# Kernel tuning notes

Measured on AMD Instinct MI355X. Metric: run time of the kernel, lower is better.

The kernel has to match this reference:

```python
import jax, jax.numpy as jnp
import numpy as np

D_MODEL = 1024
N_HEADS = 16
D_HEAD = 64
SEQ = 2048
BATCH = 2
ATTN_SCALE = float(np.sqrt(D_HEAD))  # cfg.use_attn_scale = True
NEG_INF = -1e9


def setup_inputs() -> dict:
    key = jax.random.key(0)
    ks = jax.random.split(key, 8)
    s = 0.02
    return {
        "query_input": jax.random.normal(ks[0], (BATCH, SEQ, D_MODEL), jnp.float32),
        "key_input": jax.random.normal(ks[1], (BATCH, SEQ, D_MODEL), jnp.float32),
        "value_input": jax.random.normal(ks[2], (BATCH, SEQ, D_MODEL), jnp.float32),
        "W_Q": jax.random.normal(ks[3], (N_HEADS, D_MODEL, D_HEAD), jnp.float32) * s,
        "W_K": jax.random.normal(ks[4], (N_HEADS, D_MODEL, D_HEAD), jnp.float32) * s,
        "W_V": jax.random.normal(ks[5], (N_HEADS, D_MODEL, D_HEAD), jnp.float32) * s,
        "W_O": jax.random.normal(ks[6], (N_HEADS, D_HEAD, D_MODEL), jnp.float32) * s,
        "b_Q": jnp.zeros((N_HEADS, D_HEAD), jnp.float32),
        "b_K": jnp.zeros((N_HEADS, D_HEAD), jnp.float32),
        "b_V": jnp.zeros((N_HEADS, D_HEAD), jnp.float32),
        "b_O": jnp.zeros((D_MODEL,), jnp.float32),
    }


def reference(query_input, key_input, value_input, W_Q, W_K, W_V, W_O, b_Q, b_K, b_V, b_O):
    # QKV projections: [batch, pos, d_model] x [head, d_model, d_head] -> [batch, pos, head, d_head]
    q = jnp.einsum("bpd,hde->bphe", query_input, W_Q) + b_Q
    k = jnp.einsum("bpd,hde->bphe", key_input, W_K) + b_K
    v = jnp.einsum("bpd,hde->bphe", value_input, W_V) + b_V

    # attn scores [batch, head, query_pos, key_pos]
    scores = jnp.einsum("bqhe,bkhe->bhqk", q, k) / ATTN_SCALE

    # causal mask (attn_type == 'global'): tril over [n_ctx, n_ctx] sliced to seq
    causal = jnp.tril(jnp.ones((SEQ, SEQ), bool))
    scores = jnp.where(causal[None, None, :, :], scores, NEG_INF)

    pattern = jax.nn.softmax(scores, axis=-1)

    # z: [batch, query_pos, head, d_head]
    z = jnp.einsum("bhqk,bkhe->bqhe", pattern, v)

    # output projection: [batch, pos, d_model]
    out = jnp.einsum("bqhe,hed->bqd", z, W_O) + b_O
    return out
```

## Files before the change

kernel.cpp:

```cpp
#include <hip/hip_runtime.h>
#include <stdint.h>


typedef __attribute__((ext_vector_type(8))) short short8;
typedef __attribute__((ext_vector_type(4))) short short4v;
typedef __attribute__((ext_vector_type(4))) float floatx4;
typedef __attribute__((ext_vector_type(4))) unsigned int uintx4;
typedef __attribute__((ext_vector_type(2))) unsigned int uint2v;

#define MFMA16(a, b, c) __builtin_amdgcn_mfma_f32_16x16x32_bf16(a, b, c, 0, 0, 0)

#if __has_builtin(__builtin_amdgcn_mfma_f32_16x16x16bf16_1k)
#define HAVE_K16 1
#define MFMAK16(a, b, c) __builtin_amdgcn_mfma_f32_16x16x16bf16_1k(a, b, c, 0, 0, 0)
#else
#define HAVE_K16 0
#endif

__device__ __forceinline__ unsigned short f2b(float f) {
  unsigned int u = __builtin_bit_cast(unsigned int, f);
  u = (u + 0x7fffu + ((u >> 16) & 1u)) >> 16;
  return (unsigned short)u;
}
__device__ __forceinline__ float exp2f_fast(float x) {
#if __has_builtin(__builtin_amdgcn_exp2f)
  return __builtin_amdgcn_exp2f(x);
#else
  return exp2f(x);
#endif
}
__device__ __forceinline__ unsigned int pack2_bf16(float lo, float hi) {
#if __has_builtin(__builtin_amdgcn_perm)
  return __builtin_amdgcn_perm(__builtin_bit_cast(unsigned int, hi),
                               __builtin_bit_cast(unsigned int, lo), 0x07060302u);
#else
  return (__builtin_bit_cast(unsigned int, lo) >> 16) |
         (__builtin_bit_cast(unsigned int, hi) & 0xffff0000u);
#endif
}

__device__ __forceinline__ void async_copy16(void* lds, const void* g) {
  __builtin_amdgcn_global_load_lds(
      (const __attribute__((address_space(1))) unsigned int*)g,
      (__attribute__((address_space(3))) unsigned int*)lds, 16, 0, 0);
}

__device__ __forceinline__ void xpose4(floatx4& v, int lane) {
  {
    float s0 = __shfl_xor(v[1], 1, 64);
    float s1 = __shfl_xor(v[0], 1, 64);
    float s2 = __shfl_xor(v[3], 1, 64);
    float s3 = __shfl_xor(v[2], 1, 64);
    if (lane & 1) { v[0] = s0; v[2] = s2; } else { v[1] = s1; v[3] = s3; }
  }
  {
    float s0 = __shfl_xor(v[2], 2, 64);
    float s1 = __shfl_xor(v[3], 2, 64);
    float s2 = __shfl_xor(v[0], 2, 64);
    float s3 = __shfl_xor(v[1], 2, 64);
    if (lane & 2) { v[0] = s0; v[1] = s1; } else { v[2] = s2; v[3] = s3; }
  }
}

__global__ __launch_bounds__(256) void convall(
    const float* __restrict__ Xq, const float* __restrict__ Xk,
    const float* __restrict__ Xv, const float* __restrict__ WQ,
    const float* __restrict__ WK, const float* __restrict__ WV,
    const float* __restrict__ WO, unsigned short* __restrict__ xout,
    unsigned short* __restrict__ wout, unsigned short* __restrict__ woout) {
  __shared__ float T[64][65];
  const int bid = blockIdx.x;
  const int t = threadIdx.x;
  if (bid < 12288) {
    const int yy = bid / 4096, x = bid - yy * 4096;
    const float* in = (yy == 0) ? Xq : ((yy == 1) ? Xk : Xv);
    size_t i = (size_t)x * 256 + t;
    float4 v = ((const float4*)in)[i];
    ushort4 u;
    u.x = f2b(v.x); u.y = f2b(v.y); u.z = f2b(v.z); u.w = f2b(v.w);
    ((ushort4*)(xout + (size_t)yy * 4194304))[i] = u;
    return;
  }
  const int rr = t >> 4, cc = t & 15;
  if (bid < 13056) {
    const int sub = bid - 12288;
    const int yy = sub >> 8, x = sub & 255;
    const float* in = (yy == 0) ? WQ : ((yy == 1) ? WK : WV);
    const int h = x >> 4, d0 = (x & 15) << 6;
#pragma unroll
    for (int it = 0; it < 4; ++it) {
      int dl = it * 16 + rr;
      float4 v = *(const float4*)&in[(size_t)h * 65536 + (size_t)(d0 + dl) * 64 + cc * 4];
      T[dl][cc * 4 + 0] = v.x; T[dl][cc * 4 + 1] = v.y;
      T[dl][cc * 4 + 2] = v.z; T[dl][cc * 4 + 3] = v.w;
    }
    __syncthreads();
    unsigned short* ob = wout + (size_t)yy * 1048576;
#pragma unroll
    for (int it = 0; it < 4; ++it) {
      int e = it * 16 + rr;
      ushort4 u;
      u.x = f2b(T[cc * 4 + 0][e]); u.y = f2b(T[cc * 4 + 1][e]);
      u.z = f2b(T[cc * 4 + 2][e]); u.w = f2b(T[cc * 4 + 3][e]);
      *(ushort4*)&ob[(size_t)(h * 64 + e) * 1024 + d0 + cc * 4] = u;
    }
    return;
  }
  {
    const int x = bid - 13056;
    const int r0 = (x & 15) << 6, c0 = (x >> 4) << 6;
#pragma unroll
    for (int it = 0; it < 4; ++it) {
      int rl = it * 16 + rr;
      float4 v = *(const float4*)&WO[(size_t)(r0 + rl) * 1024 + c0 + cc * 4];
      T[rl][cc * 4 + 0] = v.x; T[rl][cc * 4 + 1] = v.y;
      T[rl][cc * 4 + 2] = v.z; T[rl][cc * 4 + 3] = v.w;
    }
    __syncthreads();
#pragma unroll
    for (int it = 0; it < 4; ++it) {
      int dl = it * 16 + rr;
      ushort4 u;
      u.x = f2b(T[cc * 4 + 0][dl]); u.y = f2b(T[cc * 4 + 1][dl]);
      u.z = f2b(T[cc * 4 + 2][dl]); u.w = f2b(T[cc * 4 + 3][dl]);
      *(ushort4*)&woout[(size_t)(c0 + dl) * 1024 + r0 + cc * 4] = u;
    }
  }
}

template <int TM, int NZ>
__global__ __launch_bounds__(512, (TM == 128) ? 6 : 4) void gemm512(
    const short* __restrict__ A0, const short* __restrict__ A1,
    const short* __restrict__ A2, const short* __restrict__ B0,
    const short* __restrict__ B1, const short* __restrict__ B2,
    const float* __restrict__ bias0, const float* __restrict__ bias1,
    const float* __restrict__ bias2, unsigned short* __restrict__ ob0,
    unsigned short* __restrict__ ob1, unsigned short* __restrict__ ob2,
    float* __restrict__ outf, float qscale) {
  constexpr int WAVES_N = (TM == 128) ? 2 : 4;
  constexpr int NJ = (TM == 128) ? 4 : 2;
  constexpr int NY = 4096 / TM;
  __shared__ short As[TM * 32];
  __shared__ short Bs[128 * 32];

  const int L = blockIdx.x;
  const int x = L / (NY * NZ);
  const int r = L - x * (NY * NZ);
  const int y = r / NZ;
  const int z = r - y * NZ;

  const short* A = (z == 0) ? A0 : (z == 1) ? A1 : A2;
  const short* Bt = (z == 0) ? B0 : (z == 1) ? B1 : B2;

  const int tid = threadIdx.x;
  const int lane = tid & 63, w = tid >> 6;
  const int quad = lane >> 4, col = lane & 15;
  const int m0 = y * TM, n0 = x * 128;
  const int wm = (w / WAVES_N) * 32, wn = (w % WAVES_N) * (NJ * 16);

  floatx4 acc[2][NJ] = {};

  const int lr = lane >> 2, gc = (lane & 3) ^ ((lane >> 3) & 3);
  const short* ga = A + (size_t)(m0 + w * 16 + lr) * 1024 + gc * 8;
  const short* gb = Bt + (size_t)(n0 + w * 16 + lr) * 1024 + gc * 8;
  const int asw = (col >> 1) & 3;
  const bool stageA = (w < TM / 16);

  for (int k0 = 0; k0 < 1024; k0 += 32) {
    if (stageA) async_copy16(&As[(w * 16) * 32], ga);
    async_copy16(&Bs[(w * 16) * 32], gb);
    ga += 32; gb += 32;
    __syncthreads();
    short8 af[2], bf[NJ];
#pragma unroll
    for (int mi = 0; mi < 2; ++mi)
      af[mi] = *(const short8*)&As[(wm + mi * 16 + col) * 32 + ((quad ^ asw) * 8)];
#pragma unroll
    for (int nj = 0; nj < NJ; ++nj)
      bf[nj] = *(const short8*)&Bs[(wn + nj * 16 + col) * 32 + ((quad ^ asw) * 8)];
#pragma unroll
    for (int mi = 0; mi < 2; ++mi)
#pragma unroll
      for (int nj = 0; nj < NJ; ++nj)
        acc[mi][nj] = MFMA16(af[mi], bf[nj], acc[mi][nj]);
    __syncthreads();
  }

  const float* bias = (z == 0) ? bias0 : (z == 1) ? bias1 : bias2;
  unsigned short* outb = (z == 0) ? ob0 : (z == 1) ? ob1 : ob2;
  const int mode = (NZ == 3) ? ((z == 2) ? 2 : 1) : 0;
  const float scale = (NZ == 3 && z == 0) ? qscale : 1.0f;

  float bv[NJ];
#pragma unroll
  for (int nj = 0; nj < NJ; ++nj) bv[nj] = bias[n0 + wn + nj * 16 + col];

  if (mode == 2) {
#pragma unroll
    for (int mi = 0; mi < 2; ++mi)
#pragma unroll
      for (int nj = 0; nj < NJ; ++nj) {
        int m = m0 + wm + mi * 16 + quad * 4;
        int n = n0 + wn + nj * 16 + col;
        int bb = m >> 11, s = m & 2047, h = n >> 6, e = n & 63;
        ushort4 u;
        u.x = f2b(acc[mi][nj][0] + bv[nj]);
        u.y = f2b(acc[mi][nj][1] + bv[nj]);
        u.z = f2b(acc[mi][nj][2] + bv[nj]);
        u.w = f2b(acc[mi][nj][3] + bv[nj]);
        *(ushort4*)&outb[(((size_t)bb * 16 + h) * 64 + e) * 2048 + s] = u;
      }
  } else {
#pragma unroll
    for (int mi = 0; mi < 2; ++mi)
#pragma unroll
      for (int nj = 0; nj < NJ; ++nj) {
        floatx4 v;
#pragma unroll
        for (int rr = 0; rr < 4; ++rr) v[rr] = (acc[mi][nj][rr] + bv[nj]) * scale;
        xpose4(v, lane);
        int m = m0 + wm + mi * 16 + quad * 4 + (col & 3);
        int nb = n0 + wn + nj * 16 + (col & ~3);
        if (mode == 0) {
          *(floatx4*)&outf[(size_t)m * 1024 + nb] = v;
        } else {
          int bb = m >> 11, s = m & 2047, h = nb >> 6, e = nb & 63;
          ushort4 u;
          u.x = f2b(v[0]); u.y = f2b(v[1]); u.z = f2b(v[2]); u.w = f2b(v[3]);
          *(ushort4*)&outb[(((size_t)bb * 16 + h) * 2048 + s) * 64 + e] = u;
        }
      }
  }
}

#if !HAVE_K16
__device__ __forceinline__ void exchange4(const unsigned int* u01,
                                          const unsigned int* u23, int srcA,
                                          int srcB, bool hiq, short8& pf0,
                                          short8& pf1) {
  unsigned int xA0 = (unsigned int)__shfl((int)u01[0], srcA, 64);
  unsigned int xA1 = (unsigned int)__shfl((int)u01[1], srcA, 64);
  unsigned int yA0 = (unsigned int)__shfl((int)u23[0], srcA, 64);
  unsigned int yA1 = (unsigned int)__shfl((int)u23[1], srcA, 64);
  unsigned int xB0 = (unsigned int)__shfl((int)u01[0], srcB, 64);
  unsigned int xB1 = (unsigned int)__shfl((int)u01[1], srcB, 64);
  unsigned int yB0 = (unsigned int)__shfl((int)u23[0], srcB, 64);
  unsigned int yB1 = (unsigned int)__shfl((int)u23[1], srcB, 64);
  uintx4 v0;
  v0.x = hiq ? xA1 : xA0; v0.y = hiq ? yA1 : yA0;
  v0.z = hiq ? xB1 : xB0; v0.w = hiq ? yB1 : yB0;
  pf0 = __builtin_bit_cast(short8, v0);
  xA0 = (unsigned int)__shfl((int)u01[2], srcA, 64);
  xA1 = (unsigned int)__shfl((int)u01[3], srcA, 64);
  yA0 = (unsigned int)__shfl((int)u23[2], srcA, 64);
  yA1 = (unsigned int)__shfl((int)u23[3], srcA, 64);
  xB0 = (unsigned int)__shfl((int)u01[2], srcB, 64);
  xB1 = (unsigned int)__shfl((int)u01[3], srcB, 64);
  yB0 = (unsigned int)__shfl((int)u23[2], srcB, 64);
  yB1 = (unsigned int)__shfl((int)u23[3], srcB, 64);
  uintx4 v1;
  v1.x = hiq ? xA1 : xA0; v1.y = hiq ? yA1 : yA0;
  v1.z = hiq ? xB1 : xB0; v1.w = hiq ? yB1 : yB0;
  pf1 = __builtin_bit_cast(short8, v1);
}
#endif

__device__ __forceinline__ void stage_kv(short* Kbuf, short* Vbuf,
                                         const short* kg, const short* vg,
                                         int kv0, int w, int slr, int sgc) {
  const short* kr = kg + (size_t)(kv0 + w * 16 + slr) * 64 + sgc * 8;
  async_copy16(&Kbuf[(w * 16) * 64], kr);
  async_copy16(&Kbuf[(w * 16 + 8) * 64], kr + 8 * 64);
  const short* vr = vg + (size_t)(w * 16 + slr) * 2048 + kv0 + sgc * 8;
  async_copy16(&Vbuf[(w * 16) * 64], vr);
  async_copy16(&Vbuf[(w * 16 + 8) * 64], vr + 8 * 2048);
}

__global__ __launch_bounds__(256) void attn(const short* __restrict__ q,
                                            const short* __restrict__ k,
                                            const short* __restrict__ vt,
                                            unsigned short* __restrict__ z) {
  __shared__ short Ks[2][64 * 64];
  __shared__ short Vs[2][64 * 64];

  const int tid = threadIdx.x;
  const int lane = tid & 63, w = tid >> 6;
  const int quad = lane >> 4, col = lane & 15;
  const int qt = 31 - (blockIdx.x >> 5), bh = blockIdx.x & 31;
  const int q0 = qt * 64, qw0 = q0 + w * 16;
  const size_t base = (size_t)bh * (2048 * 64);

  const short* qp = q + base + (size_t)(qw0 + col) * 64 + quad * 8;
  short8 bq0 = *(const short8*)qp;
  short8 bq1 = *(const short8*)(qp + 32);

  floatx4 o[4] = {};
  float m_run = -1e30f, l_run = 0.f;

  const short* kg = k + base;
  const short* vg = vt + base;
  const int ksw = col & 7;
  const int slr = lane >> 3, sgc = (lane & 7) ^ slr;
#if !HAVE_K16
  const int srcA = ((quad & 1) << 5) + col, srcB = srcA + 16;
  const bool hiq = (quad & 2) != 0;
#endif

  stage_kv(Ks[0], Vs[0], kg, vg, 0, w, slr, sgc);
  int p = 0;

  for (int t = 0; t <= qt; ++t) {
    __syncthreads();
    if (t < qt) stage_kv(Ks[p ^ 1], Vs[p ^ 1], kg, vg, (t + 1) * 64, w, slr, sgc);

    const bool diag = (t == qt);
    const int mtmax = diag ? w : 3;

    floatx4 st[4];
#pragma unroll
    for (int mt = 0; mt < 4; ++mt) {
      if (mt <= mtmax) {
        const short* kb = &Ks[p][(mt * 16 + col) * 64];
        short8 ka0 = *(const short8*)(kb + (quad ^ ksw) * 8);
        short8 ka1 = *(const short8*)(kb + ((quad + 4) ^ ksw) * 8);
        floatx4 a = {0.f, 0.f, 0.f, 0.f};
        a = MFMA16(ka0, bq0, a);
        a = MFMA16(ka1, bq1, a);
        if (diag && mt == mtmax) {
#pragma unroll
          for (int r = 0; r < 4; ++r)
            if (quad * 4 + r > col) a[r] = -1e9f;
        }
        st[mt] = a;
      }
    }

    float pmax = -3e38f;
#pragma unroll
    for (int mt = 0; mt < 4; ++mt)
      if (mt <= mtmax) {
#pragma unroll
        for (int r = 0; r < 4; ++r) pmax = fmaxf(pmax, st[mt][r]);
      }
    pmax = fmaxf(pmax, __shfl_xor(pmax, 16, 64));
    pmax = fmaxf(pmax, __shfl_xor(pmax, 32, 64));
    float mnew = fmaxf(m_run, pmax);
    float alpha = exp2f_fast(m_run - mnew);
    m_run = mnew;

    unsigned int u01[4], u23[4];
    float lsum = 0.f;
#pragma unroll
    for (int mt = 0; mt < 4; ++mt) {
      if (mt <= mtmax) {
        float p0 = exp2f_fast(st[mt][0] - mnew);
        float p1 = exp2f_fast(st[mt][1] - mnew);
        float p2 = exp2f_fast(st[mt][2] - mnew);
        float p3 = exp2f_fast(st[mt][3] - mnew);
        lsum += (p0 + p1) + (p2 + p3);
        u01[mt] = pack2_bf16(p0, p1);
        u23[mt] = pack2_bf16(p2, p3);
      } else {
        u01[mt] = 0u; u23[mt] = 0u;
      }
    }
    lsum += __shfl_xor(lsum, 16, 64);
    lsum += __shfl_xor(lsum, 32, 64);
    l_run = l_run * alpha + lsum;

#if HAVE_K16
    short4v pb[4];
#pragma unroll
    for (int mt = 0; mt < 4; ++mt) {
      uint2v uu;
      uu.x = u01[mt]; uu.y = u23[mt];
      pb[mt] = __builtin_bit_cast(short4v, uu);
    }
#pragma unroll
    for (int et = 0; et < 4; ++et) {
      const short* vrow = &Vs[p][(et * 16 + col) * 64];
      floatx4 t0 = o[et];
#pragma unroll
      for (int r = 0; r < 4; ++r) t0[r] *= alpha;
#pragma unroll
      for (int mt = 0; mt < 4; ++mt) {
        if (mt <= mtmax) {
          int c = mt * 2 + (quad >> 1);
          short4v va = *(const short4v*)&vrow[((c ^ ksw) * 8) + (quad & 1) * 4];
          t0 = MFMAK16(va, pb[mt], t0);
        }
      }
      o[et] = t0;
    }
#else
    short8 pf0, pf1;
    exchange4(u01, u23, srcA, srcB, hiq, pf0, pf1);
#pragma unroll
    for (int et = 0; et < 4; ++et) {
      const short* vb = &Vs[p][(et * 16 + col) * 64];
      short8 va0 = *(const short8*)(vb + (quad ^ ksw) * 8);
      short8 va1 = *(const short8*)(vb + ((quad + 4) ^ ksw) * 8);
      floatx4 t0 = o[et];
#pragma unroll
      for (int r = 0; r < 4; ++r) t0[r] *= alpha;
      t0 = MFMA16(va0, pf0, t0);
      t0 = MFMA16(va1, pf1, t0);
      o[et] = t0;
    }
#endif
    p ^= 1;
  }

  const int b = bh >> 4, h = bh & 15;
#if __has_builtin(__builtin_amdgcn_rcpf)
  const float invl = __builtin_amdgcn_rcpf(l_run);
#else
  const float invl = 1.f / l_run;
#endif
  unsigned short* zr = z + (((size_t)b * 2048 + qw0 + col) * 16 + h) * 64;
#pragma unroll
  for (int et = 0; et < 4; ++et) {
    ushort4 u;
    u.x = f2b(o[et][0] * invl); u.y = f2b(o[et][1] * invl);
    u.z = f2b(o[et][2] * invl); u.w = f2b(o[et][3] * invl);
    *(ushort4*)&zr[et * 16 + quad * 4] = u;
  }
}

extern "C" void kernel_launch(void* const* d_in, const int* in_sizes, int n_in,
                              void* d_out, int out_size, void* d_ws, size_t ws_size,
                              hipStream_t stream) {
  (void)in_sizes; (void)n_in; (void)out_size; (void)ws_size;
  const float* Xq = (const float*)d_in[0];
  const float* Xk = (const float*)d_in[1];
  const float* Xv = (const float*)d_in[2];
  const float* WQ = (const float*)d_in[3];
  const float* WK = (const float*)d_in[4];
  const float* WV = (const float*)d_in[5];
  const float* WO = (const float*)d_in[6];
  const float* bQ = (const float*)d_in[7];
  const float* bK = (const float*)d_in[8];
  const float* bV = (const float*)d_in[9];
  const float* bO = (const float*)d_in[10];
  float* out = (float*)d_out;

  unsigned short* xqb = (unsigned short*)d_ws;
  unsigned short* xkb = xqb + 4194304;
  unsigned short* xvb = xkb + 4194304;
  unsigned short* wqt = xvb + 4194304;
  unsigned short* wkt = wqt + 1048576;
  unsigned short* wvt = wkt + 1048576;
  unsigned short* wot = wvt + 1048576;
  unsigned short* qb = wot + 1048576;
  unsigned short* kb = qb + 4194304;
  unsigned short* vtb = kb + 4194304;
  unsigned short* zb = vtb + 4194304;

  convall<<<13312, 256, 0, stream>>>(Xq, Xk, Xv, WQ, WK, WV, WO, xqb, wqt, wot);

  const float qscale = 0.125f * 1.44269504088896f;
  gemm512<128, 3><<<768, 512, 0, stream>>>(
      (const short*)xqb, (const short*)xkb, (const short*)xvb,
      (const short*)wqt, (const short*)wkt, (const short*)wvt, bQ, bK, bV, qb,
      kb, vtb, nullptr, qscale);

  attn<<<1024, 256, 0, stream>>>((const short*)qb, (const short*)kb,
                                 (const short*)vtb, zb);

  gemm512<64, 1><<<512, 512, 0, stream>>>(
      (const short*)zb, (const short*)zb, (const short*)zb, (const short*)wot,
      (const short*)wot, (const short*)wot, bO, bO, bO, nullptr, nullptr,
      nullptr, out, 1.0f);
}
```

Baseline: 218.9 us.

## Pair causal query tiles per block to share K/V staging and balance work

Each attention block now processes two query tiles (pr and 31-pr) of the same head, so every block covers 33 KV steps and work is balanced across the causal triangle. The staged K/V tiles are reused by both query tiles, which roughly halves K/V shared-memory loads per query. It also skips the online-softmax rescale when the running max does not change for the whole wavefront. The cost is halving the grid to 512 blocks and higher register pressure from two accumulator sets, which may reduce occupancy.

```diff
diff --git a/kernel.cpp b/kernel.cpp
--- a/kernel.cpp
+++ b/kernel.cpp
@@ -276,6 +276,117 @@
   async_copy16(&Vbuf[(w * 16 + 8) * 64], vr + 8 * 2048);
 }
 
+__device__ __forceinline__ void attn_step(const short* __restrict__ Kp,
+                                          const short* __restrict__ Vp,
+                                          const short8& bq0, const short8& bq1,
+                                          floatx4 (&o)[4], float& m_run,
+                                          float& l_run, int mtmax, bool diag) {
+  const int lane = threadIdx.x & 63;
+  const int quad = lane >> 4, col = lane & 15;
+  const int ksw = col & 7;
+
+  floatx4 st[4];
+#pragma unroll
+  for (int mt = 0; mt < 4; ++mt) {
+    if (mt <= mtmax) {
+      const short* kb = &Kp[(mt * 16 + col) * 64];
+      short8 ka0 = *(const short8*)(kb + (quad ^ ksw) * 8);
+      short8 ka1 = *(const short8*)(kb + ((quad + 4) ^ ksw) * 8);
+      floatx4 a = {0.f, 0.f, 0.f, 0.f};
+      a = MFMA16(ka0, bq0, a);
+      a = MFMA16(ka1, bq1, a);
+      if (diag && mt == mtmax) {
+#pragma unroll
+        for (int r = 0; r < 4; ++r)
+          if (quad * 4 + r > col) a[r] = -1e9f;
+      }
+      st[mt] = a;
+    }
+  }
+
+  float pmax = -3e38f;
+#pragma unroll
+  for (int mt = 0; mt < 4; ++mt)
+    if (mt <= mtmax) {
+#pragma unroll
+      for (int r = 0; r < 4; ++r) pmax = fmaxf(pmax, st[mt][r]);
+    }
+  pmax = fmaxf(pmax, __shfl_xor(pmax, 16, 64));
+  pmax = fmaxf(pmax, __shfl_xor(pmax, 32, 64));
+
+  const bool norescale = (__all(pmax <= m_run) != 0);
+  const float mnew = norescale ? m_run : fmaxf(m_run, pmax);
+  const float alpha = norescale ? 1.0f : exp2f_fast(m_run - mnew);
+  m_run = mnew;
+
+  unsigned int u01[4], u23[4];
+  float lsum = 0.f;
+#pragma unroll
+  for (int mt = 0; mt < 4; ++mt) {
+    if (mt <= mtmax) {
+      float p0 = exp2f_fast(st[mt][0] - mnew);
+      float p1 = exp2f_fast(st[mt][1] - mnew);
+      float p2 = exp2f_fast(st[mt][2] - mnew);
+      float p3 = exp2f_fast(st[mt][3] - mnew);
+      lsum += (p0 + p1) + (p2 + p3);
+      u01[mt] = pack2_bf16(p0, p1);
+      u23[mt] = pack2_bf16(p2, p3);
+    } else {
+      u01[mt] = 0u; u23[mt] = 0u;
+    }
+  }
+  lsum += __shfl_xor(lsum, 16, 64);
+  lsum += __shfl_xor(lsum, 32, 64);
+  l_run = norescale ? (l_run + lsum) : (l_run * alpha + lsum);
+
+#if HAVE_K16
+  short4v pb[4];
+#pragma unroll
+  for (int mt = 0; mt < 4; ++mt) {
+    uint2v uu;
+    uu.x = u01[mt]; uu.y = u23[mt];
+    pb[mt] = __builtin_bit_cast(short4v, uu);
+  }
+#pragma unroll
+  for (int et = 0; et < 4; ++et) {
+    const short* vrow = &Vp[(et * 16 + col) * 64];
+    floatx4 t0 = o[et];
+    if (!norescale) {
+#pragma unroll
+      for (int r = 0; r < 4; ++r) t0[r] *= alpha;
+    }
+#pragma unroll
+    for (int mt = 0; mt < 4; ++mt) {
+      if (mt <= mtmax) {
+        int c = mt * 2 + (quad >> 1);
+        short4v va = *(const short4v*)&vrow[((c ^ ksw) * 8) + (quad & 1) * 4];
+        t0 = MFMAK16(va, pb[mt], t0);
+      }
+    }
+    o[et] = t0;
+  }
+#else
+  const int srcA = ((quad & 1) << 5) + col, srcB = srcA + 16;
+  const bool hiq = (quad & 2) != 0;
+  short8 pf0, pf1;
+  exchange4(u01, u23, srcA, srcB, hiq, pf0, pf1);
+#pragma unroll
+  for (int et = 0; et < 4; ++et) {
+    const short* vb = &Vp[(et * 16 + col) * 64];
+    short8 va0 = *(const short8*)(vb + (quad ^ ksw) * 8);
+    short8 va1 = *(const short8*)(vb + ((quad + 4) ^ ksw) * 8);
+    floatx4 t0 = o[et];
+    if (!norescale) {
+#pragma unroll
+      for (int r = 0; r < 4; ++r) t0[r] *= alpha;
+    }
+    t0 = MFMA16(va0, pf0, t0);
+    t0 = MFMA16(va1, pf1, t0);
+    o[et] = t0;
+  }
+#endif
+}
+
 __global__ __launch_bounds__(256) void attn(const short* __restrict__ q,
                                             const short* __restrict__ k,
                                             const short* __restrict__ vt,
@@ -286,144 +397,66 @@
   const int tid = threadIdx.x;
   const int lane = tid & 63, w = tid >> 6;
   const int quad = lane >> 4, col = lane & 15;
-  const int qt = 31 - (blockIdx.x >> 5), bh = blockIdx.x & 31;
-  const int q0 = qt * 64, qw0 = q0 + w * 16;
+
+  const int bb = blockIdx.x;
+  const int bh = bb & 31;
+  const int pr = (bb < 256) ? (bb >> 5) : (15 - ((bb - 256) >> 5));
+  const int qtA = pr, qtB = 31 - pr;
+  const int q0A = qtA * 64, q0B = qtB * 64;
   const size_t base = (size_t)bh * (2048 * 64);
 
-  const short* qp = q + base + (size_t)(qw0 + col) * 64 + quad * 8;
-  short8 bq0 = *(const short8*)qp;
-  short8 bq1 = *(const short8*)(qp + 32);
-
-  floatx4 o[4] = {};
-  float m_run = -1e30f, l_run = 0.f;
+  const short* qpA = q + base + (size_t)(q0A + w * 16 + col) * 64 + quad * 8;
+  short8 bq0A = *(const short8*)qpA;
+  short8 bq1A = *(const short8*)(qpA + 32);
+  const short* qpB = q + base + (size_t)(q0B + w * 16 + col) * 64 + quad * 8;
+  short8 bq0B = *(const short8*)qpB;
+  short8 bq1B = *(const short8*)(qpB + 32);
+
+  floatx4 oA[4] = {}, oB[4] = {};
+  float mA = -1e30f, lA = 0.f;
+  float mB = -1e30f, lB = 0.f;
 
   const short* kg = k + base;
   const short* vg = vt + base;
-  const int ksw = col & 7;
   const int slr = lane >> 3, sgc = (lane & 7) ^ slr;
-#if !HAVE_K16
-  const int srcA = ((quad & 1) << 5) + col, srcB = srcA + 16;
-  const bool hiq = (quad & 2) != 0;
-#endif
 
   stage_kv(Ks[0], Vs[0], kg, vg, 0, w, slr, sgc);
   int p = 0;
 
-  for (int t = 0; t <= qt; ++t) {
+  for (int t = 0; t <= qtB; ++t) {
     __syncthreads();
-    if (t < qt) stage_kv(Ks[p ^ 1], Vs[p ^ 1], kg, vg, (t + 1) * 64, w, slr, sgc);
-
-    const bool diag = (t == qt);
-    const int mtmax = diag ? w : 3;
-
-    floatx4 st[4];
-#pragma unroll
-    for (int mt = 0; mt < 4; ++mt) {
-      if (mt <= mtmax) {
-        const short* kb = &Ks[p][(mt * 16 + col) * 64];
-        short8 ka0 = *(const short8*)(kb + (quad ^ ksw) * 8);
-        short8 ka1 = *(const short8*)(kb + ((quad + 4) ^ ksw) * 8);
-        floatx4 a = {0.f, 0.f, 0.f, 0.f};
-        a = MFMA16(ka0, bq0, a);
-        a = MFMA16(ka1, bq1, a);
-        if (diag && mt == mtmax) {
-#pragma unroll
-          for (int r = 0; r < 4; ++r)
-            if (quad * 4 + r > col) a[r] = -1e9f;
-        }
-        st[mt] = a;
-      }
-    }
-
-    float pmax = -3e38f;
-#pragma unroll
-    for (int mt = 0; mt < 4; ++mt)
-      if (mt <= mtmax) {
-#pragma unroll
-        for (int r = 0; r < 4; ++r) pmax = fmaxf(pmax, st[mt][r]);
-      }
-    pmax = fmaxf(pmax, __shfl_xor(pmax, 16, 64));
-    pmax = fmaxf(pmax, __shfl_xor(pmax, 32, 64));
-    float mnew = fmaxf(m_run, pmax);
-    float alpha = exp2f_fast(m_run - mnew);
-    m_run = mnew;
-
-    unsigned int u01[4], u23[4];
-    float lsum = 0.f;
-#pragma unroll
-    for (int mt = 0; mt < 4; ++mt) {
-      if (mt <= mtmax) {
-        float p0 = exp2f_fast(st[mt][0] - mnew);
-        float p1 = exp2f_fast(st[mt][1] - mnew);
-        float p2 = exp2f_fast(st[mt][2] - mnew);
-        float p3 = exp2f_fast(st[mt][3] - mnew);
-        lsum += (p0 + p1) + (p2 + p3);
-        u01[mt] = pack2_bf16(p0, p1);
-        u23[mt] = pack2_bf16(p2, p3);
-      } else {
-        u01[mt] = 0u; u23[mt] = 0u;
-      }
-    }
-    lsum += __shfl_xor(lsum, 16, 64);
-    lsum += __shfl_xor(lsum, 32, 64);
-    l_run = l_run * alpha + lsum;
-
-#if HAVE_K16
-    short4v pb[4];
-#pragma unroll
-    for (int mt = 0; mt < 4; ++mt) {
-      uint2v uu;
-      uu.x = u01[mt]; uu.y = u23[mt];
-      pb[mt] = __builtin_bit_cast(short4v, uu);
-    }
-#pragma unroll
-    for (int et = 0; et < 4; ++et) {
-      const short* vrow = &Vs[p][(et * 16 + col) * 64];
-      floatx4 t0 = o[et];
-#pragma unroll
-      for (int r = 0; r < 4; ++r) t0[r] *= alpha;
-#pragma unroll
-      for (int mt = 0; mt < 4; ++mt) {
-        if (mt <= mtmax) {
-          int c = mt * 2 + (quad >> 1);
-          short4v va = *(const short4v*)&vrow[((c ^ ksw) * 8) + (quad & 1) * 4];
-          t0 = MFMAK16(va, pb[mt], t0);
-        }
-      }
-      o[et] = t0;
-    }
-#else
-    short8 pf0, pf1;
-    exchange4(u01, u23, srcA, srcB, hiq, pf0, pf1);
-#pragma unroll
-    for (int et = 0; et < 4; ++et) {
-      const short* vb = &Vs[p][(et * 16 + col) * 64];
-      short8 va0 = *(const short8*)(vb + (quad ^ ksw) * 8);
-      short8 va1 = *(const short8*)(vb + ((quad + 4) ^ ksw) * 8);
-      floatx4 t0 = o[et];
-#pragma unroll
-      for (int r = 0; r < 4; ++r) t0[r] *= alpha;
-      t0 = MFMA16(va0, pf0, t0);
-      t0 = MFMA16(va1, pf1, t0);
-      o[et] = t0;
-    }
-#endif
+    if (t < qtB) stage_kv(Ks[p ^ 1], Vs[p ^ 1], kg, vg, (t + 1) * 64, w, slr, sgc);
+
+    if (t <= qtA)
+      attn_step(Ks[p], Vs[p], bq0A, bq1A, oA, mA, lA, (t == qtA) ? w : 3,
+                t == qtA);
+    attn_step(Ks[p], Vs[p], bq0B, bq1B, oB, mB, lB, (t == qtB) ? w : 3,
+              t == qtB);
     p ^= 1;
   }
 
   const int b = bh >> 4, h = bh & 15;
 #if __has_builtin(__builtin_amdgcn_rcpf)
-  const float invl = __builtin_amdgcn_rcpf(l_run);
+  const float invlA = __builtin_amdgcn_rcpf(lA);
+  const float invlB = __builtin_amdgcn_rcpf(lB);
 #else
-  const float invl = 1.f / l_run;
+  const float invlA = 1.f / lA;
+  const float invlB = 1.f / lB;
 #endif
-  unsigned short* zr = z + (((size_t)b * 2048 + qw0 + col) * 16 + h) * 64;
+  unsigned short* zrA =
+      z + (((size_t)b * 2048 + q0A + w * 16 + col) * 16 + h) * 64;
+  unsigned short* zrB =
+      z + (((size_t)b * 2048 + q0B + w * 16 + col) * 16 + h) * 64;
 #pragma unroll
   for (int et = 0; et < 4; ++et) {
-    ushort4 u;
-    u.x = f2b(o[et][0] * invl); u.y = f2b(o[et][1] * invl);
-    u.z = f2b(o[et][2] * invl); u.w = f2b(o[et][3] * invl);
-    *(ushort4*)&zr[et * 16 + quad * 4] = u;
+    ushort4 uA;
+    uA.x = f2b(oA[et][0] * invlA); uA.y = f2b(oA[et][1] * invlA);
+    uA.z = f2b(oA[et][2] * invlA); uA.w = f2b(oA[et][3] * invlA);
+    *(ushort4*)&zrA[et * 16 + quad * 4] = uA;
+    ushort4 uB;
+    uB.x = f2b(oB[et][0] * invlB); uB.y = f2b(oB[et][1] * invlB);
+    uB.z = f2b(oB[et][2] * invlB); uB.w = f2b(oB[et][3] * invlB);
+    *(ushort4*)&zrB[et * 16 + quad * 4] = uB;
   }
 }
 
@@ -464,8 +497,8 @@
       (const short*)wqt, (const short*)wkt, (const short*)wvt, bQ, bK, bV, qb,
       kb, vtb, nullptr, qscale);
 
-  attn<<<1024, 256, 0, stream>>>((const short*)qb, (const short*)kb,
-                                 (const short*)vtb, zb);
+  attn<<<512, 256, 0, stream>>>((const short*)qb, (const short*)kb,
+                                (const short*)vtb, zb);
 
   gemm512<64, 1><<<512, 512, 0, stream>>>(
       (const short*)zb, (const short*)zb, (const short*)zb, (const short*)wot,
```

Result: slower. 228.8 us (+4.5%).

## Split long causal query tiles across two blocks and merge with combine kernel

Applied to the files above, without the earlier changes.

Query tiles in the upper half of the sequence are split into two key-range halves, each processed by its own block writing fp32 partial outputs and running max/sum. A new combine kernel merges the two partials into the bf16 z buffer. Short tiles are paired with the second half of long tiles so block workloads are balanced. Blocks also skip the rescale multiply when the running max does not grow. The change adds a kernel launch and partial-result traffic through reused workspace buffers.

```diff
diff --git a/kernel.cpp b/kernel.cpp
--- a/kernel.cpp
+++ b/kernel.cpp
@@ -276,17 +276,149 @@
   async_copy16(&Vbuf[(w * 16 + 8) * 64], vr + 8 * 2048);
 }
 
+__device__ __forceinline__ void attn_step(const short* __restrict__ Kp,
+                                          const short* __restrict__ Vp,
+                                          const short8& bq0, const short8& bq1,
+                                          floatx4 (&o)[4], float& m_run,
+                                          float& l_run, int mtmax, bool diag) {
+  const int lane = threadIdx.x & 63;
+  const int quad = lane >> 4, col = lane & 15;
+  const int ksw = col & 7;
+
+  floatx4 st[4];
+#pragma unroll
+  for (int mt = 0; mt < 4; ++mt) {
+    if (mt <= mtmax) {
+      const short* kb = &Kp[(mt * 16 + col) * 64];
+      short8 ka0 = *(const short8*)(kb + (quad ^ ksw) * 8);
+      short8 ka1 = *(const short8*)(kb + ((quad + 4) ^ ksw) * 8);
+      floatx4 a = {0.f, 0.f, 0.f, 0.f};
+      a = MFMA16(ka0, bq0, a);
+      a = MFMA16(ka1, bq1, a);
+      if (diag && mt == mtmax) {
+#pragma unroll
+        for (int r = 0; r < 4; ++r)
+          if (quad * 4 + r > col) a[r] = -1e9f;
+      }
+      st[mt] = a;
+    }
+  }
+
+  float pmax = -3e38f;
+#pragma unroll
+  for (int mt = 0; mt < 4; ++mt)
+    if (mt <= mtmax) {
+#pragma unroll
+      for (int r = 0; r < 4; ++r) pmax = fmaxf(pmax, st[mt][r]);
+    }
+  pmax = fmaxf(pmax, __shfl_xor(pmax, 16, 64));
+  pmax = fmaxf(pmax, __shfl_xor(pmax, 32, 64));
+
+  const bool norescale = (__all(pmax <= m_run) != 0);
+  const float mnew = norescale ? m_run : fmaxf(m_run, pmax);
+  const float alpha = norescale ? 1.0f : exp2f_fast(m_run - mnew);
+  m_run = mnew;
+
+  unsigned int u01[4], u23[4];
+  float lsum = 0.f;
+#pragma unroll
+  for (int mt = 0; mt < 4; ++mt) {
+    if (mt <= mtmax) {
+      float p0 = exp2f_fast(st[mt][0] - mnew);
+      float p1 = exp2f_fast(st[mt][1] - mnew);
+      float p2 = exp2f_fast(st[mt][2] - mnew);
+      float p3 = exp2f_fast(st[mt][3] - mnew);
+      lsum += (p0 + p1) + (p2 + p3);
+      u01[mt] = pack2_bf16(p0, p1);
+      u23[mt] = pack2_bf16(p2, p3);
+    } else {
+      u01[mt] = 0u; u23[mt] = 0u;
+    }
+  }
+  lsum += __shfl_xor(lsum, 16, 64);
+  lsum += __shfl_xor(lsum, 32, 64);
+  l_run = norescale ? (l_run + lsum) : (l_run * alpha + lsum);
+
+#if HAVE_K16
+  short4v pb[4];
+#pragma unroll
+  for (int mt = 0; mt < 4; ++mt) {
+    uint2v uu;
+    uu.x = u01[mt]; uu.y = u23[mt];
+    pb[mt] = __builtin_bit_cast(short4v, uu);
+  }
+#pragma unroll
+  for (int et = 0; et < 4; ++et) {
+    const short* vrow = &Vp[(et * 16 + col) * 64];
+    floatx4 t0 = o[et];
+    if (!norescale) {
+#pragma unroll
+      for (int r = 0; r < 4; ++r) t0[r] *= alpha;
+    }
+#pragma unroll
+    for (int mt = 0; mt < 4; ++mt) {
+      if (mt <= mtmax) {
+        int c = mt * 2 + (quad >> 1);
+        short4v va = *(const short4v*)&vrow[((c ^ ksw) * 8) + (quad & 1) * 4];
+        t0 = MFMAK16(va, pb[mt], t0);
+      }
+    }
+    o[et] = t0;
+  }
+#else
+  const int srcA = ((quad & 1) << 5) + col, srcB = srcA + 16;
+  const bool hiq = (quad & 2) != 0;
+  short8 pf0, pf1;
+  exchange4(u01, u23, srcA, srcB, hiq, pf0, pf1);
+#pragma unroll
+  for (int et = 0; et < 4; ++et) {
+    const short* vb = &Vp[(et * 16 + col) * 64];
+    short8 va0 = *(const short8*)(vb + (quad ^ ksw) * 8);
+    short8 va1 = *(const short8*)(vb + ((quad + 4) ^ ksw) * 8);
+    floatx4 t0 = o[et];
+    if (!norescale) {
+#pragma unroll
+      for (int r = 0; r < 4; ++r) t0[r] *= alpha;
+    }
+    t0 = MFMA16(va0, pf0, t0);
+    t0 = MFMA16(va1, pf1, t0);
+    o[et] = t0;
+  }
+#endif
+}
+
 __global__ __launch_bounds__(256) void attn(const short* __restrict__ q,
                                             const short* __restrict__ k,
                                             const short* __restrict__ vt,
-                                            unsigned short* __restrict__ z) {
+                                            unsigned short* __restrict__ z,
+                                            float* __restrict__ part_o,
+                                            float* __restrict__ part_ml) {
   __shared__ short Ks[2][64 * 64];
   __shared__ short Vs[2][64 * 64];
 
   const int tid = threadIdx.x;
   const int lane = tid & 63, w = tid >> 6;
   const int quad = lane >> 4, col = lane & 15;
-  const int qt = 31 - (blockIdx.x >> 5), bh = blockIdx.x & 31;
+
+  const int bb = blockIdx.x;
+  const int bh = bb & 31;
+  int qt, ts, te, slot;
+  bool partial;
+  if (bb < 512) {
+    qt = 31 - (bb >> 5);
+    ts = 0; te = 15; partial = true; slot = (qt - 16) * 2;
+  } else {
+    const int u = bb - 512;
+    const int seg = u >> 5;
+    const int kk = 16 - (seg >> 1);
+    if ((seg & 1) == 0) {
+      qt = kk + 15; ts = 16; te = qt; partial = true; slot = (qt - 16) * 2 + 1;
+    } else {
+      qt = kk - 1; ts = 0; te = qt; partial = false; slot = 0;
+    }
+  }
+  const bool hasdiag = (te == qt);
+
   const int q0 = qt * 64, qw0 = q0 + w * 16;
   const size_t base = (size_t)bh * (2048 * 64);
 
@@ -299,116 +431,30 @@
 
   const short* kg = k + base;
   const short* vg = vt + base;
-  const int ksw = col & 7;
   const int slr = lane >> 3, sgc = (lane & 7) ^ slr;
-#if !HAVE_K16
-  const int srcA = ((quad & 1) << 5) + col, srcB = srcA + 16;
-  const bool hiq = (quad & 2) != 0;
-#endif
-
-  stage_kv(Ks[0], Vs[0], kg, vg, 0, w, slr, sgc);
+
+  stage_kv(Ks[0], Vs[0], kg, vg, ts * 64, w, slr, sgc);
   int p = 0;
 
-  for (int t = 0; t <= qt; ++t) {
+  for (int t = ts; t <= te; ++t) {
     __syncthreads();
-    if (t < qt) stage_kv(Ks[p ^ 1], Vs[p ^ 1], kg, vg, (t + 1) * 64, w, slr, sgc);
-
-    const bool diag = (t == qt);
-    const int mtmax = diag ? w : 3;
-
-    floatx4 st[4];
-#pragma unroll
-    for (int mt = 0; mt < 4; ++mt) {
-      if (mt <= mtmax) {
-        const short* kb = &Ks[p][(mt * 16 + col) * 64];
-        short8 ka0 = *(const short8*)(kb + (quad ^ ksw) * 8);
-        short8 ka1 = *(const short8*)(kb + ((quad + 4) ^ ksw) * 8);
-        floatx4 a = {0.f, 0.f, 0.f, 0.f};
-        a = MFMA16(ka0, bq0, a);
-        a = MFMA16(ka1, bq1, a);
-        if (diag && mt == mtmax) {
-#pragma unroll
-          for (int r = 0; r < 4; ++r)
-            if (quad * 4 + r > col) a[r] = -1e9f;
-        }
-        st[mt] = a;
-      }
-    }
-
-    float pmax = -3e38f;
-#pragma unroll
-    for (int mt = 0; mt < 4; ++mt)
-      if (mt <= mtmax) {
-#pragma unroll
-        for (int r = 0; r < 4; ++r) pmax = fmaxf(pmax, st[mt][r]);
-      }
-    pmax = fmaxf(pmax, __shfl_xor(pmax, 16, 64));
-    pmax = fmaxf(pmax, __shfl_xor(pmax, 32, 64));
-    float mnew = fmaxf(m_run, pmax);
-    float alpha = exp2f_fast(m_run - mnew);
-    m_run = mnew;
-
-    unsigned int u01[4], u23[4];
-    float lsum = 0.f;
-#pragma unroll
-    for (int mt = 0; mt < 4; ++mt) {
-      if (mt <= mtmax) {
-        float p0 = exp2f_fast(st[mt][0] - mnew);
-        float p1 = exp2f_fast(st[mt][1] - mnew);
-        float p2 = exp2f_fast(st[mt][2] - mnew);
-        float p3 = exp2f_fast(st[mt][3] - mnew);
-        lsum += (p0 + p1) + (p2 + p3);
-        u01[mt] = pack2_bf16(p0, p1);
-        u23[mt] = pack2_bf16(p2, p3);
-      } else {
-        u01[mt] = 0u; u23[mt] = 0u;
-      }
-    }
-    lsum += __shfl_xor(lsum, 16, 64);
-    lsum += __shfl_xor(lsum, 32, 64);
-    l_run = l_run * alpha + lsum;
-
-#if HAVE_K16
-    short4v pb[4];
-#pragma unroll
-    for (int mt = 0; mt < 4; ++mt) {
-      uint2v uu;
-      uu.x = u01[mt]; uu.y = u23[mt];
-      pb[mt] = __builtin_bit_cast(short4v, uu);
-    }
-#pragma unroll
-    for (int et = 0; et < 4; ++et) {
-      const short* vrow = &Vs[p][(et * 16 + col) * 64];
-      floatx4 t0 = o[et];
-#pragma unroll
-      for (int r = 0; r < 4; ++r) t0[r] *= alpha;
-#pragma unroll
-      for (int mt = 0; mt < 4; ++mt) {
-        if (mt <= mtmax) {
-          int c = mt * 2 + (quad >> 1);
-          short4v va = *(const short4v*)&vrow[((c ^ ksw) * 8) + (quad & 1) * 4];
-          t0 = MFMAK16(va, pb[mt], t0);
-        }
-      }
-      o[et] = t0;
-    }
-#else
-    short8 pf0, pf1;
-    exchange4(u01, u23, srcA, srcB, hiq, pf0, pf1);
-#pragma unroll
-    for (int et = 0; et < 4; ++et) {
-      const short* vb = &Vs[p][(et * 16 + col) * 64];
-      short8 va0 = *(const short8*)(vb + (quad ^ ksw) * 8);
-      short8 va1 = *(const short8*)(vb + ((quad + 4) ^ ksw) * 8);
-      floatx4 t0 = o[et];
-#pragma unroll
-      for (int r = 0; r < 4; ++r) t0[r] *= alpha;
-      t0 = MFMA16(va0, pf0, t0);
-      t0 = MFMA16(va1, pf1, t0);
-      o[et] = t0;
-    }
-#endif
+    if (t < te) stage_kv(Ks[p ^ 1], Vs[p ^ 1], kg, vg, (t + 1) * 64, w, slr, sgc);
+    const bool diag = hasdiag && (t == te);
+    attn_step(Ks[p], Vs[p], bq0, bq1, o, m_run, l_run, diag ? w : 3, diag);
     p ^= 1;
+  }
+
+  if (partial) {
+    float* po = part_o + ((size_t)slot * 32 + bh) * 4096 + (size_t)(w * 16 + col) * 64;
+#pragma unroll
+    for (int et = 0; et < 4; ++et)
+      *(floatx4*)&po[et * 16 + quad * 4] = o[et];
+    if (quad == 0) {
+      float* pm = part_ml + ((size_t)slot * 32 + bh) * 128 + (w * 16 + col) * 2;
+      pm[0] = m_run;
+      pm[1] = l_run;
+    }
+    return;
   }
 
   const int b = bh >> 4, h = bh & 15;
@@ -424,6 +470,46 @@
     u.x = f2b(o[et][0] * invl); u.y = f2b(o[et][1] * invl);
     u.z = f2b(o[et][2] * invl); u.w = f2b(o[et][3] * invl);
     *(ushort4*)&zr[et * 16 + quad * 4] = u;
+  }
+}
+
+__global__ __launch_bounds__(256) void attn_combine(
+    const float* __restrict__ part_o, const float* __restrict__ part_ml,
+    unsigned short* __restrict__ z) {
+  const int qt = 16 + (blockIdx.x >> 5), bh = blockIdx.x & 31;
+  const int sA = ((qt - 16) * 2) * 32 + bh;
+  const int sB = ((qt - 16) * 2 + 1) * 32 + bh;
+  const int t = threadIdx.x;
+  const int r = t >> 2, c0 = (t & 3) * 16;
+
+  const float* mlA = part_ml + (size_t)sA * 128 + r * 2;
+  const float* mlB = part_ml + (size_t)sB * 128 + r * 2;
+  const float mA = mlA[0], lA = mlA[1];
+  const float mB = mlB[0], lB = mlB[1];
+  const float mS = fmaxf(mA, mB);
+  const float aA = exp2f_fast(mA - mS), aB = exp2f_fast(mB - mS);
+  const float l = aA * lA + aB * lB;
+#if __has_builtin(__builtin_amdgcn_rcpf)
+  const float invl = __builtin_amdgcn_rcpf(l);
+#else
+  const float invl = 1.f / l;
+#endif
+  const float fA = aA * invl, fB = aB * invl;
+
+  const float* oA = part_o + (size_t)sA * 4096 + r * 64 + c0;
+  const float* oB = part_o + (size_t)sB * 4096 + r * 64 + c0;
+  const int b = bh >> 4, h = bh & 15;
+  unsigned short* zr = z + (((size_t)b * 2048 + qt * 64 + r) * 16 + h) * 64 + c0;
+#pragma unroll
+  for (int j = 0; j < 16; j += 4) {
+    float4 a = *(const float4*)&oA[j];
+    float4 c = *(const float4*)&oB[j];
+    ushort4 u;
+    u.x = f2b(a.x * fA + c.x * fB);
+    u.y = f2b(a.y * fA + c.y * fB);
+    u.z = f2b(a.z * fA + c.z * fB);
+    u.w = f2b(a.w * fA + c.w * fB);
+    *(ushort4*)&zr[j] = u;
   }
 }
 
@@ -456,6 +542,9 @@
   unsigned short* vtb = kb + 4194304;
   unsigned short* zb = vtb + 4194304;
 
+  float* part_o = (float*)xqb;
+  float* part_ml = (float*)xvb;
+
   convall<<<13312, 256, 0, stream>>>(Xq, Xk, Xv, WQ, WK, WV, WO, xqb, wqt, wot);
 
   const float qscale = 0.125f * 1.44269504088896f;
@@ -464,8 +553,10 @@
       (const short*)wqt, (const short*)wkt, (const short*)wvt, bQ, bK, bV, qb,
       kb, vtb, nullptr, qscale);
 
-  attn<<<1024, 256, 0, stream>>>((const short*)qb, (const short*)kb,
-                                 (const short*)vtb, zb);
+  attn<<<1536, 256, 0, stream>>>((const short*)qb, (const short*)kb,
+                                 (const short*)vtb, zb, part_o, part_ml);
+
+  attn_combine<<<512, 256, 0, stream>>>(part_o, part_ml, zb);
 
   gemm512<64, 1><<<512, 512, 0, stream>>>(
       (const short*)zb, (const short*)zb, (const short*)zb, (const short*)wot,
```

Measured after the change: 231.3 us. 1.06x slower.
